# Optimization experiments

Hardware: AMD Instinct MI355X
Metric: run time of the kernel (lower is better)

Reference implementation:

```python
import jax, jax.numpy as jnp
import numpy as np

EMB = 1024
HEADS = 16
EPS = 1e-6


def setup_inputs() -> dict:
    key = jax.random.key(0)
    ks = jax.random.split(key, 12)
    B, S, D = 2, 2048, EMB
    scale = 1.0 / np.sqrt(D)
    inp = {
        "v": jax.random.normal(ks[0], (B, S, D), jnp.float32),
        "k": jax.random.normal(ks[1], (B, S, D), jnp.float32),
        "q": jax.random.normal(ks[2], (B, S, D), jnp.float32),
        "Wv": jax.random.normal(ks[3], (D, D), jnp.float32) * scale,
        "bv": jnp.zeros((D,), jnp.float32),
        "Wk": jax.random.normal(ks[4], (D, D), jnp.float32) * scale,
        "bk": jnp.zeros((D,), jnp.float32),
        "Wq": jax.random.normal(ks[5], (D, D), jnp.float32) * scale,
        "bq": jnp.zeros((D,), jnp.float32),
        "Wo": jax.random.normal(ks[6], (D, D), jnp.float32) * scale,
        "bo": jnp.zeros((D,), jnp.float32),
        "gamma": jnp.ones((D,), jnp.float32),
        "beta": jnp.zeros((D,), jnp.float32),
    }
    return inp


def reference(v, k, q, Wv, bv, Wk, bk, Wq, bq, Wo, bo, gamma, beta):
    B, S, D = q.shape
    H = HEADS
    d = D // H  # head depth

    def split_heads(x):  # [B,S,D] -> [B,H,S,d]
        return x.reshape(B, S, H, d).transpose(0, 2, 1, 3)

    V = split_heads(v @ Wv + bv)
    K = split_heads(k @ Wk + bk)
    Q = split_heads(q @ Wq + bq)

    # scaled dot-product attention (full score matrix, no mask)
    scores = jnp.einsum("bhqd,bhkd->bhqk", Q, K) / jnp.sqrt(jnp.float32(d))
    attn = jax.nn.softmax(scores, axis=-1)
    ctx = jnp.einsum("bhqk,bhkd->bhqd", attn, V)

    ctx = ctx.transpose(0, 2, 1, 3).reshape(B, S, D)
    out = ctx @ Wo + bo + q  # final dense + residual

    # LayerNormalization(epsilon=1e-6) over last axis
    mu = jnp.mean(out, axis=-1, keepdims=True)
    var = jnp.var(out, axis=-1, keepdims=True)
    return gamma * (out - mu) * jax.lax.rsqrt(var + EPS) + beta
```

## Files before the change

### kernel.cpp

```cpp
#include <hip/hip_runtime.h>
#include <hip/hip_bf16.h>
#include <math.h>

#define D_EMB 1024
#define NBATCH 2
#define SEQ 2048
#define NH 16
#define HDIM 64
#define MTOT (NBATCH*SEQ)
#define NT (SEQ/64)

typedef unsigned short u16;
typedef unsigned long long u64;
typedef __attribute__((ext_vector_type(8))) short bf16x8;
typedef __attribute__((ext_vector_type(4))) float f32x4;
typedef __attribute__((ext_vector_type(16))) float f32x16;
typedef __attribute__((ext_vector_type(4))) unsigned short u16x4;
typedef __attribute__((ext_vector_type(4))) unsigned int u32x4;

__device__ __forceinline__ u16 f2b(float f) {
  union { float f; unsigned u; } x; x.f = f;
  unsigned r = x.u + 0x7fffu + ((x.u >> 16) & 1u);
  return (u16)(r >> 16);
}
__device__ __forceinline__ float b2f(u16 u) {
  union { unsigned u; float f; } x; x.u = ((unsigned)u) << 16;
  return x.f;
}

__device__ __forceinline__ void gld_lds16(const u16* g, u16* l) {
  __builtin_amdgcn_global_load_lds(
      (const __attribute__((address_space(1))) void*)g,
      (__attribute__((address_space(3))) void*)l, 16, 0, 0);
}

__global__ __launch_bounds__(256) void convert_qkv(
    const float* __restrict__ v, const float* __restrict__ k, const float* __restrict__ q,
    u16* __restrict__ vb, u16* __restrict__ kb, u16* __restrict__ qb) {
  int idx = blockIdx.x * 256 + threadIdx.x;
  float4 a;
  u16x4 o;
  a = ((const float4*)v)[idx];
  o.x = f2b(a.x); o.y = f2b(a.y); o.z = f2b(a.z); o.w = f2b(a.w);
  ((u16x4*)vb)[idx] = o;
  a = ((const float4*)k)[idx];
  o.x = f2b(a.x); o.y = f2b(a.y); o.z = f2b(a.z); o.w = f2b(a.w);
  ((u16x4*)kb)[idx] = o;
  a = ((const float4*)q)[idx];
  o.x = f2b(a.x); o.y = f2b(a.y); o.z = f2b(a.z); o.w = f2b(a.w);
  ((u16x4*)qb)[idx] = o;
}

__global__ __launch_bounds__(256) void transpose_w(
    const float* __restrict__ Wv, const float* __restrict__ Wk,
    const float* __restrict__ Wq, const float* __restrict__ Wo,
    u16* __restrict__ Wvt, u16* __restrict__ Wkt,
    u16* __restrict__ Wqt, u16* __restrict__ Wot) {
  __shared__ float tile[32][33];
  int z = blockIdx.z;
  const float* W = (z==0) ? Wv : (z==1) ? Wk : (z==2) ? Wq : Wo;
  u16* Wt = (z==0) ? Wvt : (z==1) ? Wkt : (z==2) ? Wqt : Wot;
  int tx = threadIdx.x, ty = threadIdx.y;
  int n0 = blockIdx.x * 32, k0 = blockIdx.y * 32;
#pragma unroll
  for (int i = 0; i < 4; ++i)
    tile[ty + i*8][tx] = W[(size_t)(k0 + ty + i*8) * D_EMB + n0 + tx];
  __syncthreads();
#pragma unroll
  for (int i = 0; i < 4; ++i)
    Wt[(size_t)(n0 + ty + i*8) * D_EMB + k0 + tx] = f2b(tile[tx][ty + i*8]);
}

__device__ __forceinline__ void gemm_loop64(
    const u16* __restrict__ A, const u16* __restrict__ Bt,
    u16* lds_a, u16* lds_b, int bm, int bn, int wid, int lane,
    f32x4 acc[4][2]) {
#pragma unroll 1
  for (int kt = 0; kt < D_EMB/64; ++kt) {
    __syncthreads();
#pragma unroll
    for (int i = 0; i < 2; ++i) {
      int chunk = wid*2 + i;
      int row = chunk*8 + (lane >> 3);
      int slot = (lane & 7) ^ (row & 7);
      gld_lds16(A + (size_t)(bm*64 + row) * D_EMB + kt*64 + slot*8,
                lds_a + chunk*512);
    }
#pragma unroll
    for (int i = 0; i < 4; ++i) {
      int chunk = i*4 + wid;
      int row = chunk*8 + (lane >> 3);
      int slot = (lane & 7) ^ (row & 7);
      gld_lds16(Bt + (size_t)(bn*128 + row) * D_EMB + kt*64 + slot*8,
                lds_b + chunk*512);
    }
    __syncthreads();
#pragma unroll
    for (int st = 0; st < 2; ++st) {
      bf16x8 af[4], bfr[2];
#pragma unroll
      for (int mb = 0; mb < 4; ++mb) {
        int row = mb*16 + (lane & 15);
        int slot = (st*4 + (lane >> 4)) ^ (row & 7);
        af[mb] = *(const bf16x8*)(lds_a + row*64 + slot*8);
      }
#pragma unroll
      for (int nb = 0; nb < 2; ++nb) {
        int row = wid*32 + nb*16 + (lane & 15);
        int slot = (st*4 + (lane >> 4)) ^ (row & 7);
        bfr[nb] = *(const bf16x8*)(lds_b + row*64 + slot*8);
      }
#pragma unroll
      for (int mb = 0; mb < 4; ++mb)
#pragma unroll
        for (int nb = 0; nb < 2; ++nb)
          acc[mb][nb] = __builtin_amdgcn_mfma_f32_16x16x32_bf16(af[mb], bfr[nb], acc[mb][nb], 0, 0, 0);
    }
  }
}

__global__ __launch_bounds__(256) void gemm_qkv(
    const u16* __restrict__ vb, const u16* __restrict__ kb, const u16* __restrict__ qb,
    const u16* __restrict__ Wvt, const u16* __restrict__ Wkt, const u16* __restrict__ Wqt,
    const float* __restrict__ bv, const float* __restrict__ bk, const float* __restrict__ bq,
    u16* __restrict__ Vt, u16* __restrict__ Kh, u16* __restrict__ Qh) {
  __shared__ u16 smem[64*64 + 128*64];
  u16* lds_a = smem;
  u16* lds_b = smem + 64*64;
  const int bid = blockIdx.x;
  const int x = bid & 7, t = bid >> 3;
  const int bn = t & 7, t2 = t >> 3;
  const int bm = (t2 & 7)*8 + x, z = t2 >> 3;
  const u16* A  = (z==0) ? vb : (z==1) ? kb : qb;
  const u16* Bt = (z==0) ? Wvt : (z==1) ? Wkt : Wqt;
  const float* bias = (z==0) ? bv : (z==1) ? bk : bq;
  int tid = threadIdx.x, wid = tid >> 6, lane = tid & 63;
  f32x4 acc[4][2];
#pragma unroll
  for (int i = 0; i < 4; ++i)
#pragma unroll
    for (int j = 0; j < 2; ++j) acc[i][j] = (f32x4){0.f,0.f,0.f,0.f};
  gemm_loop64(A, Bt, lds_a, lds_b, bm, bn, wid, lane, acc);
  int g = lane >> 4, c = lane & 15;
  if (z == 0) {
    __syncthreads();
    u16* vt_tile = smem;
#pragma unroll
    for (int mb = 0; mb < 4; ++mb) {
#pragma unroll
      for (int nb = 0; nb < 2; ++nb) {
        int col_l = wid*32 + nb*16 + c;
        float bsv = bias[bn*128 + col_l];
        union { u64 u; u16 a[4]; } w;
#pragma unroll
        for (int r = 0; r < 4; ++r) w.a[r] = f2b(acc[mb][nb][r] + bsv);
        *(u64*)(vt_tile + col_l*68 + mb*16 + g*4) = w.u;
      }
    }
    __syncthreads();
    const int dd_row = tid >> 1, half = tid & 1;
    const int h = bn*2 + (dd_row >> 6), dd = dd_row & 63;
    const int b = bm >> 5, sbase = (bm & 31) * 64;
    const u16* srcl = vt_tile + dd_row*68 + half*32;
    u16* dst = Vt + (((size_t)b*NH + h)*HDIM + dd)*SEQ + sbase + half*32;
#pragma unroll
    for (int j = 0; j < 8; ++j) ((u64*)dst)[j] = ((const u64*)srcl)[j];
  } else {
    u16* Out = (z==1) ? Kh : Qh;
    const float scl = (z == 2) ? 0.18033688f : 1.0f;
#pragma unroll
    for (int mb = 0; mb < 4; ++mb) {
      int row0 = bm*64 + mb*16 + g*4;
#pragma unroll
      for (int nb = 0; nb < 2; ++nb) {
        int col = bn*128 + wid*32 + nb*16 + c;
        float bsv = bias[col];
        int h = col >> 6, dd = col & 63;
#pragma unroll
        for (int r = 0; r < 4; ++r) {
          int m = row0 + r; int b = m >> 11, s = m & (SEQ-1);
          Out[(((size_t)b*NH + h)*SEQ + s)*HDIM + dd] = f2b((acc[mb][nb][r] + bsv) * scl);
        }
      }
    }
  }
}

__global__ __launch_bounds__(256, 2) void attn_k(
    const u16* __restrict__ Qh, const u16* __restrict__ Kh,
    const u16* __restrict__ Vt, u16* __restrict__ ctx) {
  __shared__ u16 kt_lds[2][64*64];
  __shared__ u16 vt_lds[2][64*64];
  const int tid = threadIdx.x, wid = tid >> 6, lane = tid & 63;
  const int lo5 = lane & 31, hi = lane >> 5;
  const int bid = blockIdx.x;
  const int xcd = bid & 7, idx = bid >> 3;
  const int qblk = idx & 15, bhg = idx >> 4;
  const int bh = bhg * 8 + xcd;
  const int qb = qblk * 128 + wid * 32;
  const size_t base = (size_t)bh * SEQ * HDIM;

  const int srow = tid >> 3;
  const int c0 = (tid & 7) ^ (srow & 7) ^ (srow >> 3);
  const int c1 = c0 ^ 4;
  const u16* kp0 = Kh + base + (size_t)srow * HDIM + c0*8;
  const u16* kp1 = Kh + base + (size_t)(srow+32) * HDIM + c1*8;
  const u16* vp0 = Vt + base + (size_t)srow * SEQ + c0*8;
  const u16* vp1 = Vt + base + (size_t)(srow+32) * SEQ + c1*8;

  const int r7 = lo5 & 7, r3 = lo5 >> 3;
  int offs0[4], offs1[4];
#pragma unroll
  for (int t = 0; t < 4; ++t) {
    int p = (2*t + hi) ^ r7 ^ r3;
    offs0[t] = lo5*128 + p*16;
    offs1[t] = (lo5+32)*128 + (p^4)*16;
  }
  const char* ktbase = (const char*)&kt_lds[0][0];
  const char* vtbase = (const char*)&vt_lds[0][0];

  bf16x8 qf[4];
#pragma unroll
  for (int t = 0; t < 4; ++t)
    qf[t] = *(const bf16x8*)(Qh + base + (size_t)(qb + lo5)*HDIM + t*16 + hi*8);

  f32x16 z16;
#pragma unroll
  for (int i = 0; i < 16; ++i) z16[i] = 0.f;

  f32x16 o0, o1;
#pragma unroll
  for (int i = 0; i < 16; ++i) { o0[i] = 0.f; o1[i] = 0.f; }
  float lsum = 0.f;

#define STAGE(B) do { \
    gld_lds16(kp0, &kt_lds[B][wid*512]); \
    gld_lds16(kp1, &kt_lds[B][2048 + wid*512]); \
    gld_lds16(vp0, &vt_lds[B][wid*512]); \
    gld_lds16(vp1, &vt_lds[B][2048 + wid*512]); \
    kp0 += 64*HDIM; kp1 += 64*HDIM; vp0 += 64; vp1 += 64; \
  } while (0)

#define TILE(B, VMSTR, DOSTAGE) do { \
    asm volatile("s_waitcnt " VMSTR ::: "memory"); \
    __builtin_amdgcn_sched_barrier(0); \
    __builtin_amdgcn_s_barrier();             \
    __builtin_amdgcn_sched_barrier(0); \
    const char* kb_ = ktbase + (B)*8192; \
    const char* vb_ = vtbase + (B)*8192; \
    bf16x8 kf0[4], kf1[4], vf0[4], vf1[4]; \
    _Pragma("unroll") for (int t = 0; t < 4; ++t) { \
      kf0[t] = *(const bf16x8*)(kb_ + offs0[t]); \
      kf1[t] = *(const bf16x8*)(kb_ + offs1[t]); \
      vf0[t] = *(const bf16x8*)(vb_ + offs0[t]); \
      vf1[t] = *(const bf16x8*)(vb_ + offs1[t]); } \
    asm volatile("s_waitcnt lgkmcnt(0)" ::: "memory"); \
    __builtin_amdgcn_sched_barrier(0); \
    __builtin_amdgcn_s_barrier();             \
    __builtin_amdgcn_sched_barrier(0); \
    if (DOSTAGE) { STAGE(B); } \
    __builtin_amdgcn_sched_barrier(0); \
    __builtin_amdgcn_s_setprio(1); \
    f32x16 st0 = __builtin_amdgcn_mfma_f32_32x32x16_bf16(kf0[0], qf[0], z16, 0, 0, 0); \
    f32x16 st1 = __builtin_amdgcn_mfma_f32_32x32x16_bf16(kf1[0], qf[0], z16, 0, 0, 0); \
    _Pragma("unroll") for (int t = 1; t < 4; ++t) { \
      st0 = __builtin_amdgcn_mfma_f32_32x32x16_bf16(kf0[t], qf[t], st0, 0, 0, 0); \
      st1 = __builtin_amdgcn_mfma_f32_32x32x16_bf16(kf1[t], qf[t], st1, 0, 0, 0); } \
    __builtin_amdgcn_s_setprio(0); \
    _Pragma("unroll") for (int r = 0; r < 16; ++r) { \
      st0[r] = exp2f(st0[r]); st1[r] = exp2f(st1[r]); } \
    float ps = st0[0] + st0[1]; \
    _Pragma("unroll") for (int r = 2; r < 16; ++r) ps += st0[r]; \
    _Pragma("unroll") for (int r = 0; r < 16; ++r) ps += st1[r]; \
    lsum += ps; \
    bf16x8 pa[4]; \
    _Pragma("unroll") for (int ks = 0; ks < 2; ++ks) { \
      const f32x16& s_ = ks ? st1 : st0; \
      unsigned X[8]; \
      _Pragma("unroll") for (int w = 0; w < 8; ++w) { \
        float lo_f = s_[2*w], hi_f = s_[2*w + 1]; \
        asm("v_cvt_pk_bf16_f32 %0, %1, %2" : "=v"(X[w]) : "v"(lo_f), "v"(hi_f)); } \
      asm volatile("v_permlane32_swap_b32 %0, %1" : "+v"(X[0]), "+v"(X[2])); \
      asm volatile("v_permlane32_swap_b32 %0, %1" : "+v"(X[1]), "+v"(X[3])); \
      asm volatile("v_permlane32_swap_b32 %0, %1" : "+v"(X[4]), "+v"(X[6])); \
      asm volatile("v_permlane32_swap_b32 %0, %1" : "+v"(X[5]), "+v"(X[7])); \
      union { u32x4 u; bf16x8 b; } cva, cvb; \
      cva.u = (u32x4){X[0], X[1], X[2], X[3]}; \
      cvb.u = (u32x4){X[4], X[5], X[6], X[7]}; \
      pa[2*ks]   = cva.b; \
      pa[2*ks+1] = cvb.b; } \
    __builtin_amdgcn_s_setprio(1); \
    _Pragma("unroll") for (int t = 0; t < 4; ++t) { \
      o0 = __builtin_amdgcn_mfma_f32_32x32x16_bf16(pa[t], vf0[t], o0, 0, 0, 0); \
      o1 = __builtin_amdgcn_mfma_f32_32x32x16_bf16(pa[t], vf1[t], o1, 0, 0, 0); } \
    __builtin_amdgcn_s_setprio(0); \
  } while (0)

  STAGE(0);
  STAGE(1);

#pragma unroll 1
  for (int kv = 0; kv < NT - 2; kv += 2) {
    TILE(0, "vmcnt(4)", 1);
    TILE(1, "vmcnt(4)", 1);
  }
  TILE(0, "vmcnt(4)", 0);
  TILE(1, "vmcnt(0)", 0);

#undef STAGE
#undef TILE

  lsum += __shfl_xor(lsum, 32);
  float linv = 1.0f / lsum;
  const int b = bh >> 4, h = bh & 15;
#pragma unroll
  for (int r = 0; r < 16; ++r) {
    int crow = (r & 3) + 8*(r >> 2) + 4*hi;
    float lr = __int_as_float(
        __builtin_amdgcn_ds_bpermute(crow << 2, __float_as_int(linv)));
    int s = qb + crow;
    u16* row = ctx + ((size_t)(b*SEQ + s))*D_EMB + h*64;
    row[lo5]      = f2b(o0[r] * lr);
    row[32 + lo5] = f2b(o1[r] * lr);
  }
}

__global__ __launch_bounds__(256) void gemm_out(
    const u16* __restrict__ ctx, const u16* __restrict__ Wot,
    const float* __restrict__ bo, const u16* __restrict__ resid,
    u16* __restrict__ preln) {
  __shared__ u16 smem[64*64 + 128*64];
  u16* lds_a = smem;
  u16* lds_b = smem + 64*64;
  const int bid = blockIdx.x;
  const int x = bid & 7, t = bid >> 3;
  const int bn = t & 7, bm = (t >> 3)*8 + x;
  int tid = threadIdx.x, wid = tid >> 6, lane = tid & 63;
  f32x4 acc[4][2];
#pragma unroll
  for (int i = 0; i < 4; ++i)
#pragma unroll
    for (int j = 0; j < 2; ++j) acc[i][j] = (f32x4){0.f,0.f,0.f,0.f};
  gemm_loop64(ctx, Wot, lds_a, lds_b, bm, bn, wid, lane, acc);
  int g = lane >> 4, c = lane & 15;
#pragma unroll
  for (int mb = 0; mb < 4; ++mb) {
    int row0 = bm*64 + mb*16 + g*4;
#pragma unroll
    for (int nb = 0; nb < 2; ++nb) {
      int col = bn*128 + wid*32 + nb*16 + c;
      float bsv = bo[col];
#pragma unroll
      for (int r = 0; r < 4; ++r) {
        int m = row0 + r;
        float v = acc[mb][nb][r] + bsv + b2f(resid[(size_t)m*D_EMB + col]);
        preln[(size_t)m*D_EMB + col] = f2b(v);
      }
    }
  }
}

__global__ __launch_bounds__(256) void ln_k(
    const u16* __restrict__ preln, const float* __restrict__ gamma,
    const float* __restrict__ beta, float* __restrict__ out) {
  int row = blockIdx.x, tid = threadIdx.x;
  u16x4 xr = ((const u16x4*)(preln + (size_t)row*D_EMB))[tid];
  float x0 = b2f(xr.x), x1 = b2f(xr.y), x2 = b2f(xr.z), x3 = b2f(xr.w);
  float s  = x0 + x1 + x2 + x3;
  float ss = x0*x0 + x1*x1 + x2*x2 + x3*x3;
#pragma unroll
  for (int off = 32; off; off >>= 1) {
    s  += __shfl_xor(s, off);
    ss += __shfl_xor(ss, off);
  }
  __shared__ float red_s[4], red_ss[4];
  int wid = tid >> 6, lane = tid & 63;
  if (lane == 0) { red_s[wid] = s; red_ss[wid] = ss; }
  __syncthreads();
  s  = red_s[0] + red_s[1] + red_s[2] + red_s[3];
  ss = red_ss[0] + red_ss[1] + red_ss[2] + red_ss[3];
  float mu = s * (1.0f/1024.0f);
  float var = ss * (1.0f/1024.0f) - mu*mu;
  float rstd = rsqrtf(var + 1e-6f);
  float4 gm = ((const float4*)gamma)[tid];
  float4 bt = ((const float4*)beta)[tid];
  float4 y;
  y.x = (x0 - mu)*rstd*gm.x + bt.x;
  y.y = (x1 - mu)*rstd*gm.y + bt.y;
  y.z = (x2 - mu)*rstd*gm.z + bt.z;
  y.w = (x3 - mu)*rstd*gm.w + bt.w;
  ((float4*)(out + (size_t)row*D_EMB))[tid] = y;
}

extern "C" void kernel_launch(void* const* d_in, const int* in_sizes, int n_in,
                              void* d_out, int out_size, void* d_ws, size_t ws_size,
                              hipStream_t stream) {
  const float* v_in  = (const float*)d_in[0];
  const float* k_in  = (const float*)d_in[1];
  const float* q_in  = (const float*)d_in[2];
  const float* Wv    = (const float*)d_in[3];
  const float* bv    = (const float*)d_in[4];
  const float* Wk    = (const float*)d_in[5];
  const float* bk    = (const float*)d_in[6];
  const float* Wq    = (const float*)d_in[7];
  const float* bq    = (const float*)d_in[8];
  const float* Wo    = (const float*)d_in[9];
  const float* bo    = (const float*)d_in[10];
  const float* gamma = (const float*)d_in[11];
  const float* beta  = (const float*)d_in[12];
  char* ws = (char*)d_ws;

  const size_t TOKB = (size_t)MTOT * D_EMB * 2;
  const size_t WB   = (size_t)D_EMB * D_EMB * 2;
  size_t o_qb = 0;
  size_t o_kb = o_qb + TOKB;
  size_t o_vb = o_kb + TOKB;
  size_t o_wq = o_vb + TOKB;
  size_t o_wk = o_wq + WB;
  size_t o_wv = o_wk + WB;
  size_t o_wo = o_wv + WB;
  size_t o_Qh = o_wo + WB;
  size_t o_Kh = o_Qh + TOKB;
  size_t o_Vt = o_Kh + TOKB;
  size_t o_cx = o_Vt + TOKB;

  u16* qb  = (u16*)(ws + o_qb);
  u16* kb  = (u16*)(ws + o_kb);
  u16* vb  = (u16*)(ws + o_vb);
  u16* wqt = (u16*)(ws + o_wq);
  u16* wkt = (u16*)(ws + o_wk);
  u16* wvt = (u16*)(ws + o_wv);
  u16* wot = (u16*)(ws + o_wo);
  u16* Qh  = (u16*)(ws + o_Qh);
  u16* Kh  = (u16*)(ws + o_Kh);
  u16* Vt  = (u16*)(ws + o_Vt);
  u16* cx  = (u16*)(ws + o_cx);
  u16* preln = vb;

  convert_qkv<<<4096, 256, 0, stream>>>(v_in, k_in, q_in, vb, kb, qb);
  transpose_w<<<dim3(32, 32, 4), dim3(32, 8), 0, stream>>>(Wv, Wk, Wq, Wo, wvt, wkt, wqt, wot);
  gemm_qkv<<<1536, 256, 0, stream>>>(vb, kb, qb, wvt, wkt, wqt, bv, bk, bq, Vt, Kh, Qh);
  attn_k<<<512, 256, 0, stream>>>(Qh, Kh, Vt, cx);
  gemm_out<<<512, 256, 0, stream>>>(cx, wot, bo, qb, preln);
  ln_k<<<4096, 256, 0, stream>>>(preln, gamma, beta, (float*)d_out);
}
```

Measured before the change: 137.7 us.

## Load K/V fragments directly from global memory into registers, dropping LDS staging

The attention kernel stops staging 64-row K/V tiles through double-buffered LDS with barriers. Each wave now loads its own 32-key K and V fragments straight from global memory into registers, ping-ponging two register sets so loads overlap compute. This removes LDS traffic and block-wide barriers, but each of the four waves re-reads the same K/V from global/L2 instead of sharing one copy. It also raises register pressure under the 2-blocks-per-CU bound.

```diff
diff --git a/kernel.cpp b/kernel.cpp
--- a/kernel.cpp
+++ b/kernel.cpp
@@ -8,7 +8,6 @@
 #define NH 16
 #define HDIM 64
 #define MTOT (NBATCH*SEQ)
-#define NT (SEQ/64)
 
 typedef unsigned short u16;
 typedef unsigned long long u64;
@@ -189,126 +188,83 @@
 __global__ __launch_bounds__(256, 2) void attn_k(
     const u16* __restrict__ Qh, const u16* __restrict__ Kh,
     const u16* __restrict__ Vt, u16* __restrict__ ctx) {
-  __shared__ u16 kt_lds[2][64*64];
-  __shared__ u16 vt_lds[2][64*64];
   const int tid = threadIdx.x, wid = tid >> 6, lane = tid & 63;
   const int lo5 = lane & 31, hi = lane >> 5;
   const int bid = blockIdx.x;
   const int xcd = bid & 7, idx = bid >> 3;
-  const int qblk = idx & 15, bhg = idx >> 4;
+  const int qpair = idx & 15, bhg = idx >> 4;
   const int bh = bhg * 8 + xcd;
-  const int qb = qblk * 128 + wid * 32;
+  const int q0 = (qpair*4 + wid) * 32;
   const size_t base = (size_t)bh * SEQ * HDIM;
 
-  const int srow = tid >> 3;
-  const int c0 = (tid & 7) ^ (srow & 7) ^ (srow >> 3);
-  const int c1 = c0 ^ 4;
-  const u16* kp0 = Kh + base + (size_t)srow * HDIM + c0*8;
-  const u16* kp1 = Kh + base + (size_t)(srow+32) * HDIM + c1*8;
-  const u16* vp0 = Vt + base + (size_t)srow * SEQ + c0*8;
-  const u16* vp1 = Vt + base + (size_t)(srow+32) * SEQ + c1*8;
-
-  const int r7 = lo5 & 7, r3 = lo5 >> 3;
-  int offs0[4], offs1[4];
-#pragma unroll
-  for (int t = 0; t < 4; ++t) {
-    int p = (2*t + hi) ^ r7 ^ r3;
-    offs0[t] = lo5*128 + p*16;
-    offs1[t] = (lo5+32)*128 + (p^4)*16;
-  }
-  const char* ktbase = (const char*)&kt_lds[0][0];
-  const char* vtbase = (const char*)&vt_lds[0][0];
-
   bf16x8 qf[4];
 #pragma unroll
   for (int t = 0; t < 4; ++t)
-    qf[t] = *(const bf16x8*)(Qh + base + (size_t)(qb + lo5)*HDIM + t*16 + hi*8);
+    qf[t] = *(const bf16x8*)(Qh + base + (size_t)(q0 + lo5)*HDIM + t*16 + hi*8);
+
+  const u16* kp  = Kh + base + (size_t)lo5 * HDIM + hi*8;
+  const u16* vpA = Vt + base + (size_t)lo5 * SEQ + hi*8;
+  const u16* vpB = Vt + base + (size_t)(32 + lo5) * SEQ + hi*8;
 
   f32x16 z16;
 #pragma unroll
   for (int i = 0; i < 16; ++i) z16[i] = 0.f;
-
   f32x16 o0, o1;
 #pragma unroll
   for (int i = 0; i < 16; ++i) { o0[i] = 0.f; o1[i] = 0.f; }
   float lsum = 0.f;
 
-#define STAGE(B) do { \
-    gld_lds16(kp0, &kt_lds[B][wid*512]); \
-    gld_lds16(kp1, &kt_lds[B][2048 + wid*512]); \
-    gld_lds16(vp0, &vt_lds[B][wid*512]); \
-    gld_lds16(vp1, &vt_lds[B][2048 + wid*512]); \
-    kp0 += 64*HDIM; kp1 += 64*HDIM; vp0 += 64; vp1 += 64; \
+  bf16x8 kfA[4], vaA[2], vbA[2];
+  bf16x8 kfB[4], vaB[2], vbB[2];
+
+#define LOADT(KF, VA, VB, S0) do { \
+    const int s0_ = (S0);                       \
+    _Pragma("unroll") for (int ti = 0; ti < 4; ++ti) \
+      KF[ti] = *(const bf16x8*)(kp + (size_t)s0_*HDIM + ti*16); \
+    _Pragma("unroll") for (int ks = 0; ks < 2; ++ks) { \
+      VA[ks] = *(const bf16x8*)(vpA + s0_ + ks*16); \
+      VB[ks] = *(const bf16x8*)(vpB + s0_ + ks*16); } \
   } while (0)
 
-#define TILE(B, VMSTR, DOSTAGE) do { \
-    asm volatile("s_waitcnt " VMSTR ::: "memory"); \
-    __builtin_amdgcn_sched_barrier(0); \
-    __builtin_amdgcn_s_barrier();             \
-    __builtin_amdgcn_sched_barrier(0); \
-    const char* kb_ = ktbase + (B)*8192; \
-    const char* vb_ = vtbase + (B)*8192; \
-    bf16x8 kf0[4], kf1[4], vf0[4], vf1[4]; \
-    _Pragma("unroll") for (int t = 0; t < 4; ++t) { \
-      kf0[t] = *(const bf16x8*)(kb_ + offs0[t]); \
-      kf1[t] = *(const bf16x8*)(kb_ + offs1[t]); \
-      vf0[t] = *(const bf16x8*)(vb_ + offs0[t]); \
-      vf1[t] = *(const bf16x8*)(vb_ + offs1[t]); } \
-    asm volatile("s_waitcnt lgkmcnt(0)" ::: "memory"); \
-    __builtin_amdgcn_sched_barrier(0); \
-    __builtin_amdgcn_s_barrier();             \
-    __builtin_amdgcn_sched_barrier(0); \
-    if (DOSTAGE) { STAGE(B); } \
-    __builtin_amdgcn_sched_barrier(0); \
-    __builtin_amdgcn_s_setprio(1); \
-    f32x16 st0 = __builtin_amdgcn_mfma_f32_32x32x16_bf16(kf0[0], qf[0], z16, 0, 0, 0); \
-    f32x16 st1 = __builtin_amdgcn_mfma_f32_32x32x16_bf16(kf1[0], qf[0], z16, 0, 0, 0); \
-    _Pragma("unroll") for (int t = 1; t < 4; ++t) { \
-      st0 = __builtin_amdgcn_mfma_f32_32x32x16_bf16(kf0[t], qf[t], st0, 0, 0, 0); \
-      st1 = __builtin_amdgcn_mfma_f32_32x32x16_bf16(kf1[t], qf[t], st1, 0, 0, 0); } \
-    __builtin_amdgcn_s_setprio(0); \
-    _Pragma("unroll") for (int r = 0; r < 16; ++r) { \
-      st0[r] = exp2f(st0[r]); st1[r] = exp2f(st1[r]); } \
-    float ps = st0[0] + st0[1]; \
-    _Pragma("unroll") for (int r = 2; r < 16; ++r) ps += st0[r]; \
-    _Pragma("unroll") for (int r = 0; r < 16; ++r) ps += st1[r]; \
+#define COMPT(KF, VA, VB) do { \
+    f32x16 st = __builtin_amdgcn_mfma_f32_32x32x16_bf16(KF[0], qf[0], z16, 0, 0, 0); \
+    _Pragma("unroll") for (int ti = 1; ti < 4; ++ti) \
+      st = __builtin_amdgcn_mfma_f32_32x32x16_bf16(KF[ti], qf[ti], st, 0, 0, 0); \
+    _Pragma("unroll") for (int r = 0; r < 16; ++r) st[r] = exp2f(st[r]); \
+    float ps = st[0] + st[1]; \
+    _Pragma("unroll") for (int r = 2; r < 16; ++r) ps += st[r]; \
     lsum += ps; \
-    bf16x8 pa[4]; \
-    _Pragma("unroll") for (int ks = 0; ks < 2; ++ks) { \
-      const f32x16& s_ = ks ? st1 : st0; \
-      unsigned X[8]; \
-      _Pragma("unroll") for (int w = 0; w < 8; ++w) { \
-        float lo_f = s_[2*w], hi_f = s_[2*w + 1]; \
-        asm("v_cvt_pk_bf16_f32 %0, %1, %2" : "=v"(X[w]) : "v"(lo_f), "v"(hi_f)); } \
-      asm volatile("v_permlane32_swap_b32 %0, %1" : "+v"(X[0]), "+v"(X[2])); \
-      asm volatile("v_permlane32_swap_b32 %0, %1" : "+v"(X[1]), "+v"(X[3])); \
-      asm volatile("v_permlane32_swap_b32 %0, %1" : "+v"(X[4]), "+v"(X[6])); \
-      asm volatile("v_permlane32_swap_b32 %0, %1" : "+v"(X[5]), "+v"(X[7])); \
-      union { u32x4 u; bf16x8 b; } cva, cvb; \
-      cva.u = (u32x4){X[0], X[1], X[2], X[3]}; \
-      cvb.u = (u32x4){X[4], X[5], X[6], X[7]}; \
-      pa[2*ks]   = cva.b; \
-      pa[2*ks+1] = cvb.b; } \
-    __builtin_amdgcn_s_setprio(1); \
-    _Pragma("unroll") for (int t = 0; t < 4; ++t) { \
-      o0 = __builtin_amdgcn_mfma_f32_32x32x16_bf16(pa[t], vf0[t], o0, 0, 0, 0); \
-      o1 = __builtin_amdgcn_mfma_f32_32x32x16_bf16(pa[t], vf1[t], o1, 0, 0, 0); } \
-    __builtin_amdgcn_s_setprio(0); \
+    unsigned X[8]; \
+    _Pragma("unroll") for (int w = 0; w < 8; ++w) { \
+      float lo_f = st[2*w], hi_f = st[2*w + 1]; \
+      asm("v_cvt_pk_bf16_f32 %0, %1, %2" : "=v"(X[w]) : "v"(lo_f), "v"(hi_f)); } \
+    asm volatile("v_permlane32_swap_b32 %0, %1" : "+v"(X[0]), "+v"(X[2])); \
+    asm volatile("v_permlane32_swap_b32 %0, %1" : "+v"(X[1]), "+v"(X[3])); \
+    asm volatile("v_permlane32_swap_b32 %0, %1" : "+v"(X[4]), "+v"(X[6])); \
+    asm volatile("v_permlane32_swap_b32 %0, %1" : "+v"(X[5]), "+v"(X[7])); \
+    union { u32x4 u; bf16x8 b; } cva, cvb; \
+    cva.u = (u32x4){X[0], X[1], X[2], X[3]}; \
+    cvb.u = (u32x4){X[4], X[5], X[6], X[7]}; \
+    o0 = __builtin_amdgcn_mfma_f32_32x32x16_bf16(cva.b, VA[0], o0, 0, 0, 0); \
+    o0 = __builtin_amdgcn_mfma_f32_32x32x16_bf16(cvb.b, VA[1], o0, 0, 0, 0); \
+    o1 = __builtin_amdgcn_mfma_f32_32x32x16_bf16(cva.b, VB[0], o1, 0, 0, 0); \
+    o1 = __builtin_amdgcn_mfma_f32_32x32x16_bf16(cvb.b, VB[1], o1, 0, 0, 0); \
   } while (0)
 
-  STAGE(0);
-  STAGE(1);
-
+  LOADT(kfA, vaA, vbA, 0);
 #pragma unroll 1
-  for (int kv = 0; kv < NT - 2; kv += 2) {
-    TILE(0, "vmcnt(4)", 1);
-    TILE(1, "vmcnt(4)", 1);
-  }
-  TILE(0, "vmcnt(4)", 0);
-  TILE(1, "vmcnt(0)", 0);
-
-#undef STAGE
-#undef TILE
+  for (int t = 0; t < 31; ++t) {
+    LOADT(kfB, vaB, vbB, (2*t+1)*32);
+    COMPT(kfA, vaA, vbA);
+    LOADT(kfA, vaA, vbA, (2*t+2)*32);
+    COMPT(kfB, vaB, vbB);
+  }
+  LOADT(kfB, vaB, vbB, 63*32);
+  COMPT(kfA, vaA, vbA);
+  COMPT(kfB, vaB, vbB);
+
+#undef LOADT
+#undef COMPT
 
   lsum += __shfl_xor(lsum, 32);
   float linv = 1.0f / lsum;
@@ -318,7 +274,7 @@
     int crow = (r & 3) + 8*(r >> 2) + 4*hi;
     float lr = __int_as_float(
         __builtin_amdgcn_ds_bpermute(crow << 2, __float_as_int(linv)));
-    int s = qb + crow;
+    int s = q0 + crow;
     u16* row = ctx + ((size_t)(b*SEQ + s))*D_EMB + h*64;
     row[lo5]      = f2b(o0[r] * lr);
     row[32 + lo5] = f2b(o1[r] * lr);
```

Measured after the change: 198.3 us. 1.44x slower.
